# Kernel optimization log

Hardware: AMD Instinct MI355X
Metric: run time of the kernel (lower is better)

The kernel has to match this reference:

```python
import jax, jax.numpy as jnp
import numpy as np
from jax import lax

DIM = 64
B, H, W = 4, 256, 256


def setup_inputs() -> dict:
    key = jax.random.key(0)
    ks = jax.random.split(key, 6)
    d = DIM
    x = jax.random.normal(ks[0], (B, d, H, W), dtype=jnp.float32)
    w_hidden = jax.random.normal(ks[1], (6 * d, d), dtype=jnp.float32) * 0.05      # 1x1 conv dim->6*dim
    w_dw = jax.random.normal(ks[2], (6 * d, 1, 3, 3), dtype=jnp.float32) * 0.05    # depthwise 3x3
    norm_w = jnp.ones((2 * d,), dtype=jnp.float32)
    norm_b = jnp.zeros((2 * d,), dtype=jnp.float32)
    w_out = jax.random.normal(ks[3], (d, 2 * d), dtype=jnp.float32) * 0.05         # 1x1 conv 2*dim->dim
    return {"x": x, "w_hidden": w_hidden, "w_dw": w_dw,
            "norm_w": norm_w, "norm_b": norm_b, "w_out": w_out, "patch_size": 8}


def reference(x, w_hidden, w_dw, norm_w, norm_b, w_out, patch_size):
    p = patch_size
    b, c, h, w = x.shape
    # 1x1 conv: dim -> 6*dim
    hidden = jnp.einsum('oc,bchw->bohw', w_hidden, x)
    # depthwise 3x3 conv, padding=1
    hidden = lax.conv_general_dilated(
        hidden, w_dw, window_strides=(1, 1), padding='SAME',
        dimension_numbers=('NCHW', 'OIHW', 'NCHW'),
        feature_group_count=w_dw.shape[0])
    q, k, v = jnp.split(hidden, 3, axis=1)  # each [b, 2c, h, w]

    c2 = 2 * c
    def to_patch(t):  # b c (h p1) (w p2) -> b c h w p1 p2
        return t.reshape(b, c2, h // p, p, w // p, p).transpose(0, 1, 2, 4, 3, 5)

    q_fft = jnp.fft.rfft2(to_patch(q).astype(jnp.float32))
    k_fft = jnp.fft.rfft2(to_patch(k).astype(jnp.float32))
    out = jnp.fft.irfft2(q_fft * k_fft, s=(p, p))  # circular conv per patch
    # b c h w p1 p2 -> b c (h p1) (w p2)
    out = out.transpose(0, 1, 2, 4, 3, 5).reshape(b, c2, h, w)

    # WithBias LayerNorm over channel dim (to_3d normalizes last dim = channels)
    mu = out.mean(axis=1, keepdims=True)
    var = out.var(axis=1, keepdims=True)
    out_norm = (out - mu) / jnp.sqrt(var + 1e-5)
    out_norm = out_norm * norm_w[None, :, None, None] + norm_b[None, :, None, None]

    gated = v * out_norm
    # 1x1 conv: 2*dim -> dim
    return jnp.einsum('oc,bchw->bohw', w_out, gated)
```

## Files before the change

kernel.cpp:

```cpp
#include <hip/hip_runtime.h>


typedef _Float16 f16x8 __attribute__((ext_vector_type(8)));
typedef _Float16 f16x4 __attribute__((ext_vector_type(4)));
typedef _Float16 f16x2 __attribute__((ext_vector_type(2)));
typedef __fp16   h16x2 __attribute__((ext_vector_type(2)));
typedef float    f32x4 __attribute__((ext_vector_type(4)));

#define XS_OFF    0
#define HS_OFF    12800
#define QCC_OFF   25600
#define TMP_OFF   43008
#define MU_OFF    51712
#define RSTD_OFF  51968
#define LNW_OFF   52224
#define LNB_OFF   52480
#define LDS_BYTES 52736

__global__ __launch_bounds__(512, 4) void lfsa_fused(
    const float* __restrict__ x,
    const float* __restrict__ wh,
    const float* __restrict__ wdw,
    const float* __restrict__ nw,
    const float* __restrict__ nb,
    const float* __restrict__ wo,
    float* __restrict__ out)
{
    extern __shared__ char lds[];
    _Float16* xs    = (_Float16*)(lds + XS_OFF);
    _Float16* hs    = (_Float16*)(lds + HS_OFF);
    _Float16* qcc16 = (_Float16*)(lds + QCC_OFF);
    _Float16* tmp16 = (_Float16*)(lds + TMP_OFF);
    _Float16* gs16  = (_Float16*)(lds + TMP_OFF);
    float*    scrF  = (float*)(lds + TMP_OFF);
    float*    mu_s  = (float*)(lds + MU_OFF);
    float*    rstd_s= (float*)(lds + RSTD_OFF);
    _Float16* lnw16 = (_Float16*)(lds + LNW_OFF);
    _Float16* lnb16 = (_Float16*)(lds + LNB_OFF);

    const int tid = threadIdx.x;
    const int px = blockIdx.x, py = blockIdx.y, bz = blockIdx.z;
    const int lane = tid & 63;
    const int wv   = tid >> 6;
    const int m16  = lane & 15;
    const int quad = lane >> 4;

    {
        const int pix  = tid & 127;
        const int gg   = tid >> 7;
        const int prow = pix / 10;
        const int pcol = pix - prow * 10;
        const int yy = py * 8 + prow - 1;
        const int xx = px * 8 + pcol - 1;
        const bool inimg = (pix < 100) && ((unsigned)yy < 256u) && ((unsigned)xx < 256u);
        if (pix < 100) {
            const float* xp = inimg
                ? (x + (size_t)((bz * 64 + gg * 16) * 65536 + yy * 256 + xx)) : x;
            f16x8 lo, hi;
            #pragma unroll
            for (int i = 0; i < 8; ++i) {
                lo[i] = (_Float16)(inimg ? xp[(size_t)i * 65536] : 0.0f);
                hi[i] = (_Float16)(inimg ? xp[(size_t)(i + 8) * 65536] : 0.0f);
            }
            const int s = pix & 7;
            _Float16* xrow = xs + pix * 64;
            *(f16x8*)(xrow + (((2 * gg)     ^ s) * 8)) = lo;
            *(f16x8*)(xrow + (((2 * gg + 1) ^ s) * 8)) = hi;
        }
        if (tid < 128) { lnw16[tid] = (_Float16)nw[tid]; lnb16[tid] = (_Float16)nb[tid]; }
    }

    const int dwo = tid >> 3;
    const int blk = tid & 7;
    const int by2 = (blk >> 1) * 2;
    const int bx4 = (blk & 1) * 4;
    const int ci  = tid & 7;

    const int ot = wv >> 1;
    const float* wha = wh + (size_t)(ot * 16 + m16) * 64 + quad * 8;
    float4 wr0 = *(const float4*)(wha);
    float4 wr1 = *(const float4*)(wha + 4);
    float4 wr2 = *(const float4*)(wha + 32);
    float4 wr3 = *(const float4*)(wha + 36);

    f32x4 pacc2[2] = {{0.f,0.f,0.f,0.f},{0.f,0.f,0.f,0.f}};
    float sS2[8], sQ2[8];

    __syncthreads();

    #pragma unroll 1
    for (int kc = 0; kc < 6; ++kc) {
        const f16x8 a0 = {(_Float16)wr0.x,(_Float16)wr0.y,(_Float16)wr0.z,(_Float16)wr0.w,
                          (_Float16)wr1.x,(_Float16)wr1.y,(_Float16)wr1.z,(_Float16)wr1.w};
        const f16x8 a1 = {(_Float16)wr2.x,(_Float16)wr2.y,(_Float16)wr2.z,(_Float16)wr2.w,
                          (_Float16)wr3.x,(_Float16)wr3.y,(_Float16)wr3.z,(_Float16)wr3.w};
        if (kc < 5) {
            const float* nx = wha + (size_t)(kc + 1) * 4096;
            wr0 = *(const float4*)(nx);
            wr1 = *(const float4*)(nx + 4);
            wr2 = *(const float4*)(nx + 32);
            wr3 = *(const float4*)(nx + 36);
        }
        float w9c[9];
        #pragma unroll
        for (int t = 0; t < 9; ++t) w9c[t] = wdw[(kc * 64 + dwo) * 9 + t];

        {
            const int np  = (wv & 1) ? 3 : 4;
            const int pt0 = (wv & 1) * 4;
            for (int pp = 0; pp < np; ++pp) {
                const int pt = pt0 + pp;
                const int pixg = pt * 16 + m16;
                const _Float16* xrow = xs + pixg * 64;
                const int c0 = ((quad ^ (pixg & 7)) * 8);
                const f16x8 b0 = *(const f16x8*)(xrow + c0);
                const f16x8 b1 = *(const f16x8*)(xrow + (c0 ^ 32));
                f32x4 d = {0.f,0.f,0.f,0.f};
                d = __builtin_amdgcn_mfma_f32_16x16x32_f16(b0, a0, d, 0, 0, 0);
                d = __builtin_amdgcn_mfma_f32_16x16x32_f16(b1, a1, d, 0, 0, 0);
                const int pbase = pt * 16 + quad * 4;
                if (pbase < 100) {
                    *(f16x4*)(hs + 100 * (ot * 16 + m16) + pbase) =
                        f16x4{(_Float16)d[0], (_Float16)d[1],
                              (_Float16)d[2], (_Float16)d[3]};
                }
            }
        }
        __syncthreads();

        if (kc == 4) {
            if (tid < 64) {
                float S = 0.0f, Q = 0.0f;
                #pragma unroll
                for (int w = 0; w < 8; ++w) {
                    S += scrF[272 * w + tid];
                    Q += scrF[272 * w + 64 + tid];
                }
                const float sm = S * 0.0078125f;
                const float sq = Q * 0.0078125f;
                mu_s[tid]   = sm;
                rstd_s[tid] = rsqrtf(sq - sm * sm + 1e-5f);
            }
            __syncthreads();
        }

        if (kc < 4) {
            const _Float16* hrow = hs + 100 * dwo;
            float in[4][6];
            #pragma unroll
            for (int r = 0; r < 4; ++r) {
                const _Float16* rp = hrow + (by2 + r) * 10 + bx4;
                const f16x2 p0 = *(const f16x2*)rp;
                const f16x2 p1 = *(const f16x2*)(rp + 2);
                const f16x2 p2 = *(const f16x2*)(rp + 4);
                in[r][0] = (float)p0[0]; in[r][1] = (float)p0[1];
                in[r][2] = (float)p1[0]; in[r][3] = (float)p1[1];
                in[r][4] = (float)p2[0]; in[r][5] = (float)p2[1];
            }
            #pragma unroll
            for (int r = 0; r < 2; ++r) {
                float rv[4];
                #pragma unroll
                for (int c = 0; c < 4; ++c) {
                    float s = 0.0f;
                    #pragma unroll
                    for (int dy = 0; dy < 3; ++dy)
                        #pragma unroll
                        for (int dx = 0; dx < 3; ++dx)
                            s = fmaf(w9c[dy * 3 + dx], in[r + dy][c + dx], s);
                    rv[c] = s;
                }
                const int off = (by2 + r) * 8 + bx4;
                _Float16* dst = (kc < 2) ? (qcc16 + 68 * (kc * 64 + dwo))
                                         : (tmp16 + 68 * dwo);
                *(f16x4*)(dst + off) = f16x4{(_Float16)rv[0], (_Float16)rv[1],
                                             (_Float16)rv[2], (_Float16)rv[3]};
            }
        } else {
            const _Float16* hrow = hs + 100 * dwo;
            const int chg = (kc - 4) * 64 + dwo;
            const float lw = (float)lnw16[chg], lb = (float)lnb16[chg];
            const _Float16* ccrow = qcc16 + 68 * chg;
            float in[4][6];
            #pragma unroll
            for (int r = 0; r < 4; ++r) {
                const _Float16* rp = hrow + (by2 + r) * 10 + bx4;
                const f16x2 p0 = *(const f16x2*)rp;
                const f16x2 p1 = *(const f16x2*)(rp + 2);
                const f16x2 p2 = *(const f16x2*)(rp + 4);
                in[r][0] = (float)p0[0]; in[r][1] = (float)p0[1];
                in[r][2] = (float)p1[0]; in[r][3] = (float)p1[1];
                in[r][4] = (float)p2[0]; in[r][5] = (float)p2[1];
            }
            #pragma unroll
            for (int r = 0; r < 2; ++r) {
                const int prow = by2 + r;
                const f16x4 cc4 = *(const f16x4*)(ccrow + prow * 8 + bx4);
                const f32x4 mu4 = *(const f32x4*)(mu_s + prow * 8 + bx4);
                const f32x4 rs4 = *(const f32x4*)(rstd_s + prow * 8 + bx4);
                #pragma unroll
                for (int c = 0; c < 4; ++c) {
                    float s = 0.0f;
                    #pragma unroll
                    for (int dy = 0; dy < 3; ++dy)
                        #pragma unroll
                        for (int dx = 0; dx < 3; ++dx)
                            s = fmaf(w9c[dy * 3 + dx], in[r + dy][c + dx], s);
                    const float nrm = ((float)cc4[c] - mu4[c]) * rs4[c] * lw + lb;
                    gs16[(prow * 8 + bx4 + c) * 68 + dwo] = (_Float16)(s * nrm);
                }
            }
        }
        __syncthreads();

        if (kc == 2 || kc == 3) {
            const int ch = (kc - 2) * 64 + dwo;
            _Float16* qrow = qcc16 + 68 * ch;
            const _Float16* krow = tmp16 + 68 * dwo;
            float acc[8];
            #pragma unroll
            for (int j = 0; j < 8; ++j) acc[j] = 0.0f;
            #pragma unroll
            for (int a = 0; a < 8; ++a) {
                const f16x8 qv = *(const f16x8*)(qrow + 8 * a);
                h16x2 q2[4];
                #pragma unroll
                for (int t = 0; t < 4; ++t) {
                    q2[t][0] = (__fp16)qv[2 * t];
                    q2[t][1] = (__fp16)qv[2 * t + 1];
                }
                const int r = (ci - a) & 7;
                const f16x8 kr = *(const f16x8*)(krow + 8 * r);
                h16x2 rp[8];
                #pragma unroll
                for (int i = 0; i < 8; ++i)
                    rp[i] = h16x2{(__fp16)kr[i], (__fp16)kr[(i + 7) & 7]};
                #pragma unroll
                for (int j = 0; j < 8; ++j)
                    #pragma unroll
                    for (int t = 0; t < 4; ++t)
                        acc[j] = __builtin_amdgcn_fdot2(q2[t], rp[(j - 2 * t) & 7],
                                                        acc[j], false);
            }
            #pragma unroll
            for (int j = 0; j < 8; ++j) {
                float sS = acc[j];
                float sQ = acc[j] * acc[j];
                sS += __shfl_xor(sS, 8, 64);
                sQ += __shfl_xor(sQ, 8, 64);
                sS += __shfl_xor(sS, 16, 64);
                sQ += __shfl_xor(sQ, 16, 64);
                sS += __shfl_xor(sS, 32, 64);
                sQ += __shfl_xor(sQ, 32, 64);
                if (kc == 2) { sS2[j] = sS; sQ2[j] = sQ; }
                else         { sS2[j] += sS; sQ2[j] += sQ; }
            }
            *(f16x4*)(qrow + 8 * ci)     = f16x4{(_Float16)acc[0], (_Float16)acc[1],
                                                 (_Float16)acc[2], (_Float16)acc[3]};
            *(f16x4*)(qrow + 8 * ci + 4) = f16x4{(_Float16)acc[4], (_Float16)acc[5],
                                                 (_Float16)acc[6], (_Float16)acc[7]};
            if (kc == 3 && lane < 8) {
                float* w0 = scrF + 272 * wv + lane * 8;
                *(f32x4*)(w0)          = f32x4{sS2[0], sS2[1], sS2[2], sS2[3]};
                *(f32x4*)(w0 + 4)      = f32x4{sS2[4], sS2[5], sS2[6], sS2[7]};
                *(f32x4*)(w0 + 64)     = f32x4{sQ2[0], sQ2[1], sQ2[2], sQ2[3]};
                *(f32x4*)(w0 + 68)     = f32x4{sQ2[4], sQ2[5], sQ2[6], sQ2[7]};
            }
        }

        if (kc >= 4) {
            const int cb = (kc - 4) * 64;
            const float* wop = wo + (size_t)(ot * 16 + m16) * 128 + cb + quad * 8;
            const float4 u0 = *(const float4*)(wop);
            const float4 u1 = *(const float4*)(wop + 4);
            const float4 u2 = *(const float4*)(wop + 32);
            const float4 u3 = *(const float4*)(wop + 36);
            const f16x8 pa0 = {(_Float16)u0.x,(_Float16)u0.y,(_Float16)u0.z,(_Float16)u0.w,
                               (_Float16)u1.x,(_Float16)u1.y,(_Float16)u1.z,(_Float16)u1.w};
            const f16x8 pa1 = {(_Float16)u2.x,(_Float16)u2.y,(_Float16)u2.z,(_Float16)u2.w,
                               (_Float16)u3.x,(_Float16)u3.y,(_Float16)u3.z,(_Float16)u3.w};
            #pragma unroll
            for (int tt = 0; tt < 2; ++tt) {
                const int pt = (wv & 1) * 2 + tt;
                const _Float16* bp = gs16 + (pt * 16 + m16) * 68 + quad * 8;
                const f16x8 b0 = *(const f16x8*)bp;
                const f16x8 b1 = *(const f16x8*)(bp + 32);
                pacc2[tt] = __builtin_amdgcn_mfma_f32_16x16x32_f16(pa0, b0, pacc2[tt], 0, 0, 0);
                pacc2[tt] = __builtin_amdgcn_mfma_f32_16x16x32_f16(pa1, b1, pacc2[tt], 0, 0, 0);
            }
        }
    }

    {
        #pragma unroll
        for (int tt = 0; tt < 2; ++tt) {
            const int pixg = ((wv & 1) * 2 + tt) * 16 + m16;
            const int r = pixg >> 3, c = pixg & 7;
            float* op = out + (size_t)(bz * 64 + ot * 16 + quad * 4) * 65536
                            + (py * 8 + r) * 256 + px * 8 + c;
            #pragma unroll
            for (int reg = 0; reg < 4; ++reg)
                op[(size_t)reg * 65536] = pacc2[tt][reg];
        }
    }
}

extern "C" void kernel_launch(void* const* d_in, const int* in_sizes, int n_in,
                              void* d_out, int out_size, void* d_ws, size_t ws_size,
                              hipStream_t stream) {
    const float* x   = (const float*)d_in[0];
    const float* wh  = (const float*)d_in[1];
    const float* wdw = (const float*)d_in[2];
    const float* nw  = (const float*)d_in[3];
    const float* nb  = (const float*)d_in[4];
    const float* wo  = (const float*)d_in[5];
    float* outp = (float*)d_out;

    (void)hipFuncSetAttribute((const void*)lfsa_fused,
                              hipFuncAttributeMaxDynamicSharedMemorySize, LDS_BYTES);
    dim3 grid(32, 32, 4);
    lfsa_fused<<<grid, 512, LDS_BYTES, stream>>>(x, wh, wdw, nw, nb, wo, outp);
}
```

Baseline: 398.7 us.

## Hoist x fragments into registers and alias xs with qcc to shrink LDS

Loads the per-wave x B-fragments from LDS once before the kc loop and keeps them in registers, so the x staging buffer can share space with the qcc buffer. The LDS layout is repacked, cutting the per-block footprint, which may allow more resident blocks per CU. The weight prefetch across iterations is dropped in favor of in-loop loads. The cost is more VGPRs per thread and exposed global weight-load latency.

```diff
diff --git a/kernel.cpp b/kernel.cpp
--- a/kernel.cpp
+++ b/kernel.cpp
@@ -7,15 +7,14 @@
 typedef __fp16   h16x2 __attribute__((ext_vector_type(2)));
 typedef float    f32x4 __attribute__((ext_vector_type(4)));
 
-#define XS_OFF    0
-#define HS_OFF    12800
-#define QCC_OFF   25600
-#define TMP_OFF   43008
-#define MU_OFF    51712
-#define RSTD_OFF  51968
-#define LNW_OFF   52224
-#define LNB_OFF   52480
-#define LDS_BYTES 52736
+#define QCC_OFF   0
+#define TMP_OFF   17408
+#define HS_OFF    26112
+#define MU_OFF    38912
+#define RSTD_OFF  39168
+#define LNW_OFF   39424
+#define LNB_OFF   39680
+#define LDS_BYTES 39936
 
 __global__ __launch_bounds__(512, 4) void lfsa_fused(
     const float* __restrict__ x,
@@ -27,12 +26,12 @@
     float* __restrict__ out)
 {
     extern __shared__ char lds[];
-    _Float16* xs    = (_Float16*)(lds + XS_OFF);
-    _Float16* hs    = (_Float16*)(lds + HS_OFF);
+    _Float16* xs    = (_Float16*)(lds + QCC_OFF);
     _Float16* qcc16 = (_Float16*)(lds + QCC_OFF);
     _Float16* tmp16 = (_Float16*)(lds + TMP_OFF);
     _Float16* gs16  = (_Float16*)(lds + TMP_OFF);
     float*    scrF  = (float*)(lds + TMP_OFF);
+    _Float16* hs    = (_Float16*)(lds + HS_OFF);
     float*    mu_s  = (float*)(lds + MU_OFF);
     float*    rstd_s= (float*)(lds + RSTD_OFF);
     _Float16* lnw16 = (_Float16*)(lds + LNW_OFF);
@@ -78,52 +77,51 @@
 
     const int ot = wv >> 1;
     const float* wha = wh + (size_t)(ot * 16 + m16) * 64 + quad * 8;
-    float4 wr0 = *(const float4*)(wha);
-    float4 wr1 = *(const float4*)(wha + 4);
-    float4 wr2 = *(const float4*)(wha + 32);
-    float4 wr3 = *(const float4*)(wha + 36);
 
     f32x4 pacc2[2] = {{0.f,0.f,0.f,0.f},{0.f,0.f,0.f,0.f}};
     float sS2[8], sQ2[8];
 
     __syncthreads();
 
+    const int np  = (wv & 1) ? 3 : 4;
+    const int pt0 = (wv & 1) * 4;
+    f16x8 xb0[4], xb1[4];
+    #pragma unroll
+    for (int pp = 0; pp < 4; ++pp) {
+        const int pixg = (pt0 + ((pp < np) ? pp : 0)) * 16 + m16;
+        const _Float16* xrow = xs + pixg * 64;
+        const int c0 = ((quad ^ (pixg & 7)) * 8);
+        xb0[pp] = *(const f16x8*)(xrow + c0);
+        xb1[pp] = *(const f16x8*)(xrow + (c0 ^ 32));
+    }
+
     #pragma unroll 1
     for (int kc = 0; kc < 6; ++kc) {
-        const f16x8 a0 = {(_Float16)wr0.x,(_Float16)wr0.y,(_Float16)wr0.z,(_Float16)wr0.w,
-                          (_Float16)wr1.x,(_Float16)wr1.y,(_Float16)wr1.z,(_Float16)wr1.w};
-        const f16x8 a1 = {(_Float16)wr2.x,(_Float16)wr2.y,(_Float16)wr2.z,(_Float16)wr2.w,
-                          (_Float16)wr3.x,(_Float16)wr3.y,(_Float16)wr3.z,(_Float16)wr3.w};
-        if (kc < 5) {
-            const float* nx = wha + (size_t)(kc + 1) * 4096;
-            wr0 = *(const float4*)(nx);
-            wr1 = *(const float4*)(nx + 4);
-            wr2 = *(const float4*)(nx + 32);
-            wr3 = *(const float4*)(nx + 36);
-        }
+        const float* wp = wha + (size_t)kc * 4096;
+        const float4 v0 = *(const float4*)(wp);
+        const float4 v1 = *(const float4*)(wp + 4);
+        const float4 v2 = *(const float4*)(wp + 32);
+        const float4 v3 = *(const float4*)(wp + 36);
         float w9c[9];
         #pragma unroll
         for (int t = 0; t < 9; ++t) w9c[t] = wdw[(kc * 64 + dwo) * 9 + t];
-
-        {
-            const int np  = (wv & 1) ? 3 : 4;
-            const int pt0 = (wv & 1) * 4;
-            for (int pp = 0; pp < np; ++pp) {
-                const int pt = pt0 + pp;
-                const int pixg = pt * 16 + m16;
-                const _Float16* xrow = xs + pixg * 64;
-                const int c0 = ((quad ^ (pixg & 7)) * 8);
-                const f16x8 b0 = *(const f16x8*)(xrow + c0);
-                const f16x8 b1 = *(const f16x8*)(xrow + (c0 ^ 32));
-                f32x4 d = {0.f,0.f,0.f,0.f};
-                d = __builtin_amdgcn_mfma_f32_16x16x32_f16(b0, a0, d, 0, 0, 0);
-                d = __builtin_amdgcn_mfma_f32_16x16x32_f16(b1, a1, d, 0, 0, 0);
-                const int pbase = pt * 16 + quad * 4;
-                if (pbase < 100) {
-                    *(f16x4*)(hs + 100 * (ot * 16 + m16) + pbase) =
-                        f16x4{(_Float16)d[0], (_Float16)d[1],
-                              (_Float16)d[2], (_Float16)d[3]};
-                }
+        const f16x8 a0 = {(_Float16)v0.x,(_Float16)v0.y,(_Float16)v0.z,(_Float16)v0.w,
+                          (_Float16)v1.x,(_Float16)v1.y,(_Float16)v1.z,(_Float16)v1.w};
+        const f16x8 a1 = {(_Float16)v2.x,(_Float16)v2.y,(_Float16)v2.z,(_Float16)v2.w,
+                          (_Float16)v3.x,(_Float16)v3.y,(_Float16)v3.z,(_Float16)v3.w};
+
+        #pragma unroll
+        for (int pp = 0; pp < 4; ++pp) {
+            if (pp >= np) break;
+            const int pt = pt0 + pp;
+            f32x4 d = {0.f,0.f,0.f,0.f};
+            d = __builtin_amdgcn_mfma_f32_16x16x32_f16(xb0[pp], a0, d, 0, 0, 0);
+            d = __builtin_amdgcn_mfma_f32_16x16x32_f16(xb1[pp], a1, d, 0, 0, 0);
+            const int pbase = pt * 16 + quad * 4;
+            if (pbase < 100) {
+                *(f16x4*)(hs + 100 * (ot * 16 + m16) + pbase) =
+                    f16x4{(_Float16)d[0], (_Float16)d[1],
+                          (_Float16)d[2], (_Float16)d[3]};
             }
         }
         __syncthreads();
```

Measured after the change: 492.4 us. 1.23x slower.

## Double-buffer hidden tile and pipeline next-chunk GEMM with current depthwise stage

Applied to the files above, without the earlier changes.

The hidden-activation LDS buffer becomes two buffers. The 1x1-conv MFMA for channel chunk kc+1 is issued in the same barrier interval as the depthwise and elementwise work for chunk kc. The gated output gets two separate buffers, and its projection is deferred so one __syncthreads per iteration can go. This aims to cut barrier stalls and overlap matrix-core work with VALU work. In exchange, LDS use rises from about 52KB to about 74KB per block, which may lower how many blocks fit on a CU.

```diff
diff --git a/kernel.cpp b/kernel.cpp
--- a/kernel.cpp
+++ b/kernel.cpp
@@ -8,14 +8,16 @@
 typedef float    f32x4 __attribute__((ext_vector_type(4)));
 
 #define XS_OFF    0
-#define HS_OFF    12800
-#define QCC_OFF   25600
-#define TMP_OFF   43008
-#define MU_OFF    51712
-#define RSTD_OFF  51968
-#define LNW_OFF   52224
-#define LNB_OFF   52480
-#define LDS_BYTES 52736
+#define QCC_OFF   12800
+#define GS0_OFF   30208
+#define TMP_OFF   38912
+#define HS0_OFF   47616
+#define HS1_OFF   60416
+#define MU_OFF    73216
+#define RSTD_OFF  73472
+#define LNW_OFF   73728
+#define LNB_OFF   73984
+#define LDS_BYTES 74240
 
 __global__ __launch_bounds__(512, 4) void lfsa_fused(
     const float* __restrict__ x,
@@ -28,10 +30,10 @@
 {
     extern __shared__ char lds[];
     _Float16* xs    = (_Float16*)(lds + XS_OFF);
-    _Float16* hs    = (_Float16*)(lds + HS_OFF);
     _Float16* qcc16 = (_Float16*)(lds + QCC_OFF);
+    _Float16* gs0   = (_Float16*)(lds + GS0_OFF);
     _Float16* tmp16 = (_Float16*)(lds + TMP_OFF);
-    _Float16* gs16  = (_Float16*)(lds + TMP_OFF);
+    _Float16* gs1   = (_Float16*)(lds + TMP_OFF);
     float*    scrF  = (float*)(lds + TMP_OFF);
     float*    mu_s  = (float*)(lds + MU_OFF);
     float*    rstd_s= (float*)(lds + RSTD_OFF);
@@ -44,6 +46,22 @@
     const int wv   = tid >> 6;
     const int m16  = lane & 15;
     const int quad = lane >> 4;
+
+    const int dwo = tid >> 3;
+    const int blk = tid & 7;
+    const int by2 = (blk >> 1) * 2;
+    const int bx4 = (blk & 1) * 4;
+    const int ci  = tid & 7;
+
+    const int ot = wv >> 1;
+    const float* wha = wh + (size_t)(ot * 16 + m16) * 64 + quad * 8;
+    const int np  = (wv & 1) ? 3 : 4;
+    const int pt0 = (wv & 1) * 4;
+
+    float4 wr0 = *(const float4*)(wha);
+    float4 wr1 = *(const float4*)(wha + 4);
+    float4 wr2 = *(const float4*)(wha + 32);
+    float4 wr3 = *(const float4*)(wha + 36);
 
     {
         const int pix  = tid & 127;
@@ -70,63 +88,87 @@
         if (tid < 128) { lnw16[tid] = (_Float16)nw[tid]; lnb16[tid] = (_Float16)nb[tid]; }
     }
 
-    const int dwo = tid >> 3;
-    const int blk = tid & 7;
-    const int by2 = (blk >> 1) * 2;
-    const int bx4 = (blk & 1) * 4;
-    const int ci  = tid & 7;
-
-    const int ot = wv >> 1;
-    const float* wha = wh + (size_t)(ot * 16 + m16) * 64 + quad * 8;
-    float4 wr0 = *(const float4*)(wha);
-    float4 wr1 = *(const float4*)(wha + 4);
-    float4 wr2 = *(const float4*)(wha + 32);
-    float4 wr3 = *(const float4*)(wha + 36);
-
     f32x4 pacc2[2] = {{0.f,0.f,0.f,0.f},{0.f,0.f,0.f,0.f}};
     float sS2[8], sQ2[8];
 
+    auto do_gemm = [&](f16x8 a0, f16x8 a1, _Float16* hsbuf) {
+        for (int pp = 0; pp < np; ++pp) {
+            const int pt = pt0 + pp;
+            const int pixg = pt * 16 + m16;
+            const _Float16* xrow = xs + pixg * 64;
+            const int c0 = ((quad ^ (pixg & 7)) * 8);
+            const f16x8 b0 = *(const f16x8*)(xrow + c0);
+            const f16x8 b1 = *(const f16x8*)(xrow + (c0 ^ 32));
+            f32x4 d = {0.f,0.f,0.f,0.f};
+            d = __builtin_amdgcn_mfma_f32_16x16x32_f16(b0, a0, d, 0, 0, 0);
+            d = __builtin_amdgcn_mfma_f32_16x16x32_f16(b1, a1, d, 0, 0, 0);
+            const int pbase = pt * 16 + quad * 4;
+            if (pbase < 100) {
+                *(f16x4*)(hsbuf + 100 * (ot * 16 + m16) + pbase) =
+                    f16x4{(_Float16)d[0], (_Float16)d[1],
+                          (_Float16)d[2], (_Float16)d[3]};
+            }
+        }
+    };
+
+    auto do_proj = [&](const _Float16* gsbuf, int cb) {
+        const float* wop = wo + (size_t)(ot * 16 + m16) * 128 + cb + quad * 8;
+        const float4 u0 = *(const float4*)(wop);
+        const float4 u1 = *(const float4*)(wop + 4);
+        const float4 u2 = *(const float4*)(wop + 32);
+        const float4 u3 = *(const float4*)(wop + 36);
+        const f16x8 pa0 = {(_Float16)u0.x,(_Float16)u0.y,(_Float16)u0.z,(_Float16)u0.w,
+                           (_Float16)u1.x,(_Float16)u1.y,(_Float16)u1.z,(_Float16)u1.w};
+        const f16x8 pa1 = {(_Float16)u2.x,(_Float16)u2.y,(_Float16)u2.z,(_Float16)u2.w,
+                           (_Float16)u3.x,(_Float16)u3.y,(_Float16)u3.z,(_Float16)u3.w};
+        #pragma unroll
+        for (int tt = 0; tt < 2; ++tt) {
+            const int pt = (wv & 1) * 2 + tt;
+            const _Float16* bp = gsbuf + (pt * 16 + m16) * 68 + quad * 8;
+            const f16x8 b0 = *(const f16x8*)bp;
+            const f16x8 b1 = *(const f16x8*)(bp + 32);
+            pacc2[tt] = __builtin_amdgcn_mfma_f32_16x16x32_f16(pa0, b0, pacc2[tt], 0, 0, 0);
+            pacc2[tt] = __builtin_amdgcn_mfma_f32_16x16x32_f16(pa1, b1, pacc2[tt], 0, 0, 0);
+        }
+    };
+
     __syncthreads();
 
-    #pragma unroll 1
-    for (int kc = 0; kc < 6; ++kc) {
+    {
         const f16x8 a0 = {(_Float16)wr0.x,(_Float16)wr0.y,(_Float16)wr0.z,(_Float16)wr0.w,
                           (_Float16)wr1.x,(_Float16)wr1.y,(_Float16)wr1.z,(_Float16)wr1.w};
         const f16x8 a1 = {(_Float16)wr2.x,(_Float16)wr2.y,(_Float16)wr2.z,(_Float16)wr2.w,
                           (_Float16)wr3.x,(_Float16)wr3.y,(_Float16)wr3.z,(_Float16)wr3.w};
-        if (kc < 5) {
-            const float* nx = wha + (size_t)(kc + 1) * 4096;
-            wr0 = *(const float4*)(nx);
-            wr1 = *(const float4*)(nx + 4);
-            wr2 = *(const float4*)(nx + 32);
-            wr3 = *(const float4*)(nx + 36);
-        }
+        const float* nx = wha + 4096;
+        wr0 = *(const float4*)(nx);
+        wr1 = *(const float4*)(nx + 4);
+        wr2 = *(const float4*)(nx + 32);
+        wr3 = *(const float4*)(nx + 36);
+        do_gemm(a0, a1, (_Float16*)(lds + HS0_OFF));
+    }
+
+    #pragma unroll 1
+    for (int kc = 0; kc < 6; ++kc) {
+        __syncthreads();
+
         float w9c[9];
         #pragma unroll
         for (int t = 0; t < 9; ++t) w9c[t] = wdw[(kc * 64 + dwo) * 9 + t];
 
-        {
-            const int np  = (wv & 1) ? 3 : 4;
-            const int pt0 = (wv & 1) * 4;
-            for (int pp = 0; pp < np; ++pp) {
-                const int pt = pt0 + pp;
-                const int pixg = pt * 16 + m16;
-                const _Float16* xrow = xs + pixg * 64;
-                const int c0 = ((quad ^ (pixg & 7)) * 8);
-                const f16x8 b0 = *(const f16x8*)(xrow + c0);
-                const f16x8 b1 = *(const f16x8*)(xrow + (c0 ^ 32));
-                f32x4 d = {0.f,0.f,0.f,0.f};
-                d = __builtin_amdgcn_mfma_f32_16x16x32_f16(b0, a0, d, 0, 0, 0);
-                d = __builtin_amdgcn_mfma_f32_16x16x32_f16(b1, a1, d, 0, 0, 0);
-                const int pbase = pt * 16 + quad * 4;
-                if (pbase < 100) {
-                    *(f16x4*)(hs + 100 * (ot * 16 + m16) + pbase) =
-                        f16x4{(_Float16)d[0], (_Float16)d[1],
-                              (_Float16)d[2], (_Float16)d[3]};
-                }
-            }
-        }
-        __syncthreads();
+        if (kc < 5) {
+            const f16x8 a0 = {(_Float16)wr0.x,(_Float16)wr0.y,(_Float16)wr0.z,(_Float16)wr0.w,
+                              (_Float16)wr1.x,(_Float16)wr1.y,(_Float16)wr1.z,(_Float16)wr1.w};
+            const f16x8 a1 = {(_Float16)wr2.x,(_Float16)wr2.y,(_Float16)wr2.z,(_Float16)wr2.w,
+                              (_Float16)wr3.x,(_Float16)wr3.y,(_Float16)wr3.z,(_Float16)wr3.w};
+            if (kc < 4) {
+                const float* nx = wha + (size_t)(kc + 2) * 4096;
+                wr0 = *(const float4*)(nx);
+                wr1 = *(const float4*)(nx + 4);
+                wr2 = *(const float4*)(nx + 32);
+                wr3 = *(const float4*)(nx + 36);
+            }
+            do_gemm(a0, a1, (_Float16*)(lds + (((kc + 1) & 1) ? HS1_OFF : HS0_OFF)));
+        }
 
         if (kc == 4) {
             if (tid < 64) {
@@ -144,8 +186,10 @@
             __syncthreads();
         }
 
+        const _Float16* hcur = (_Float16*)(lds + ((kc & 1) ? HS1_OFF : HS0_OFF));
+
         if (kc < 4) {
-            const _Float16* hrow = hs + 100 * dwo;
+            const _Float16* hrow = hcur + 100 * dwo;
             float in[4][6];
             #pragma unroll
             for (int r = 0; r < 4; ++r) {
@@ -177,10 +221,11 @@
                                              (_Float16)rv[2], (_Float16)rv[3]};
             }
         } else {
-            const _Float16* hrow = hs + 100 * dwo;
+            const _Float16* hrow = hcur + 100 * dwo;
             const int chg = (kc - 4) * 64 + dwo;
             const float lw = (float)lnw16[chg], lb = (float)lnb16[chg];
             const _Float16* ccrow = qcc16 + 68 * chg;
+            _Float16* gsc = (kc == 4) ? gs0 : gs1;
             float in[4][6];
             #pragma unroll
             for (int r = 0; r < 4; ++r) {
@@ -207,11 +252,10 @@
                         for (int dx = 0; dx < 3; ++dx)
                             s = fmaf(w9c[dy * 3 + dx], in[r + dy][c + dx], s);
                     const float nrm = ((float)cc4[c] - mu4[c]) * rs4[c] * lw + lb;
-                    gs16[(prow * 8 + bx4 + c) * 68 + dwo] = (_Float16)(s * nrm);
+                    gsc[(prow * 8 + bx4 + c) * 68 + dwo] = (_Float16)(s * nrm);
                 }
             }
         }
-        __syncthreads();
 
         if (kc == 2 || kc == 3) {
             const int ch = (kc - 2) * 64 + dwo;
@@ -268,28 +312,14 @@
             }
         }
 
-        if (kc >= 4) {
-            const int cb = (kc - 4) * 64;
-            const float* wop = wo + (size_t)(ot * 16 + m16) * 128 + cb + quad * 8;
-            const float4 u0 = *(const float4*)(wop);
-            const float4 u1 = *(const float4*)(wop + 4);
-            const float4 u2 = *(const float4*)(wop + 32);
-            const float4 u3 = *(const float4*)(wop + 36);
-            const f16x8 pa0 = {(_Float16)u0.x,(_Float16)u0.y,(_Float16)u0.z,(_Float16)u0.w,
-                               (_Float16)u1.x,(_Float16)u1.y,(_Float16)u1.z,(_Float16)u1.w};
-            const f16x8 pa1 = {(_Float16)u2.x,(_Float16)u2.y,(_Float16)u2.z,(_Float16)u2.w,
-                               (_Float16)u3.x,(_Float16)u3.y,(_Float16)u3.z,(_Float16)u3.w};
-            #pragma unroll
-            for (int tt = 0; tt < 2; ++tt) {
-                const int pt = (wv & 1) * 2 + tt;
-                const _Float16* bp = gs16 + (pt * 16 + m16) * 68 + quad * 8;
-                const f16x8 b0 = *(const f16x8*)bp;
-                const f16x8 b1 = *(const f16x8*)(bp + 32);
-                pacc2[tt] = __builtin_amdgcn_mfma_f32_16x16x32_f16(pa0, b0, pacc2[tt], 0, 0, 0);
-                pacc2[tt] = __builtin_amdgcn_mfma_f32_16x16x32_f16(pa1, b1, pacc2[tt], 0, 0, 0);
-            }
+        if (kc == 5) {
+            do_proj(gs0, 0);
         }
     }
+
+    __syncthreads();
+
+    do_proj(gs1, 64);
 
     {
         #pragma unroll
```

Measured after the change: 399.3 us. About the same (+0.2%).

## Process 128 hidden channels per round to halve barrier-separated stages

Applied to the files above, without the earlier changes.

Restructures the six 64-channel stages into three 128-channel rounds: each wave computes a full 16-channel MFMA tile over all pixel tiles, and the depthwise, circular-convolution and gating steps each handle two channels per thread. This cuts the number of barriers and loop iterations and batches the output projection into one round. In exchange, LDS use grows from about 52KB to about 74KB, which may limit how many 512-thread blocks fit per CU (launch bounds ask for 4), and register pressure rises from the doubled weights and unrolled work.

```diff
diff --git a/kernel.cpp b/kernel.cpp
--- a/kernel.cpp
+++ b/kernel.cpp
@@ -9,13 +9,13 @@
 
 #define XS_OFF    0
 #define HS_OFF    12800
-#define QCC_OFF   25600
-#define TMP_OFF   43008
-#define MU_OFF    51712
-#define RSTD_OFF  51968
-#define LNW_OFF   52224
-#define LNB_OFF   52480
-#define LDS_BYTES 52736
+#define QCC_OFF   38400
+#define TMP_OFF   55808
+#define MU_OFF    73216
+#define RSTD_OFF  73472
+#define LNW_OFF   73728
+#define LNB_OFF   73984
+#define LDS_BYTES 74240
 
 __global__ __launch_bounds__(512, 4) void lfsa_fused(
     const float* __restrict__ x,
@@ -45,6 +45,21 @@
     const int m16  = lane & 15;
     const int quad = lane >> 4;
 
+    const int dwo = tid >> 3;
+    const int blk = tid & 7;
+    const int by2 = (blk >> 1) * 2;
+    const int bx4 = (blk & 1) * 4;
+    const int ci  = tid & 7;
+
+    const int och = wv * 16 + m16;
+    const float* wha = wh + (size_t)och * 64 + quad * 8;
+    const int ot  = wv >> 1;
+
+    float4 wr0 = *(const float4*)(wha);
+    float4 wr1 = *(const float4*)(wha + 4);
+    float4 wr2 = *(const float4*)(wha + 32);
+    float4 wr3 = *(const float4*)(wha + 36);
+
     {
         const int pix  = tid & 127;
         const int gg   = tid >> 7;
@@ -70,65 +85,49 @@
         if (tid < 128) { lnw16[tid] = (_Float16)nw[tid]; lnb16[tid] = (_Float16)nb[tid]; }
     }
 
-    const int dwo = tid >> 3;
-    const int blk = tid & 7;
-    const int by2 = (blk >> 1) * 2;
-    const int bx4 = (blk & 1) * 4;
-    const int ci  = tid & 7;
-
-    const int ot = wv >> 1;
-    const float* wha = wh + (size_t)(ot * 16 + m16) * 64 + quad * 8;
-    float4 wr0 = *(const float4*)(wha);
-    float4 wr1 = *(const float4*)(wha + 4);
-    float4 wr2 = *(const float4*)(wha + 32);
-    float4 wr3 = *(const float4*)(wha + 36);
-
     f32x4 pacc2[2] = {{0.f,0.f,0.f,0.f},{0.f,0.f,0.f,0.f}};
-    float sS2[8], sQ2[8];
 
     __syncthreads();
 
     #pragma unroll 1
-    for (int kc = 0; kc < 6; ++kc) {
+    for (int rg = 0; rg < 3; ++rg) {
         const f16x8 a0 = {(_Float16)wr0.x,(_Float16)wr0.y,(_Float16)wr0.z,(_Float16)wr0.w,
                           (_Float16)wr1.x,(_Float16)wr1.y,(_Float16)wr1.z,(_Float16)wr1.w};
         const f16x8 a1 = {(_Float16)wr2.x,(_Float16)wr2.y,(_Float16)wr2.z,(_Float16)wr2.w,
                           (_Float16)wr3.x,(_Float16)wr3.y,(_Float16)wr3.z,(_Float16)wr3.w};
-        if (kc < 5) {
-            const float* nx = wha + (size_t)(kc + 1) * 4096;
+        if (rg < 2) {
+            const float* nx = wha + (size_t)(rg + 1) * 8192;
             wr0 = *(const float4*)(nx);
             wr1 = *(const float4*)(nx + 4);
             wr2 = *(const float4*)(nx + 32);
             wr3 = *(const float4*)(nx + 36);
         }
-        float w9c[9];
+        float w9a[9], w9b[9];
         #pragma unroll
-        for (int t = 0; t < 9; ++t) w9c[t] = wdw[(kc * 64 + dwo) * 9 + t];
-
-        {
-            const int np  = (wv & 1) ? 3 : 4;
-            const int pt0 = (wv & 1) * 4;
-            for (int pp = 0; pp < np; ++pp) {
-                const int pt = pt0 + pp;
-                const int pixg = pt * 16 + m16;
-                const _Float16* xrow = xs + pixg * 64;
-                const int c0 = ((quad ^ (pixg & 7)) * 8);
-                const f16x8 b0 = *(const f16x8*)(xrow + c0);
-                const f16x8 b1 = *(const f16x8*)(xrow + (c0 ^ 32));
-                f32x4 d = {0.f,0.f,0.f,0.f};
-                d = __builtin_amdgcn_mfma_f32_16x16x32_f16(b0, a0, d, 0, 0, 0);
-                d = __builtin_amdgcn_mfma_f32_16x16x32_f16(b1, a1, d, 0, 0, 0);
-                const int pbase = pt * 16 + quad * 4;
-                if (pbase < 100) {
-                    *(f16x4*)(hs + 100 * (ot * 16 + m16) + pbase) =
-                        f16x4{(_Float16)d[0], (_Float16)d[1],
-                              (_Float16)d[2], (_Float16)d[3]};
-                }
+        for (int t = 0; t < 9; ++t) {
+            w9a[t] = wdw[(rg * 128 + dwo) * 9 + t];
+            w9b[t] = wdw[(rg * 128 + 64 + dwo) * 9 + t];
+        }
+
+        for (int pt = 0; pt < 7; ++pt) {
+            const int pixg = pt * 16 + m16;
+            const _Float16* xrow = xs + pixg * 64;
+            const int c0 = ((quad ^ (pixg & 7)) * 8);
+            const f16x8 b0 = *(const f16x8*)(xrow + c0);
+            const f16x8 b1 = *(const f16x8*)(xrow + (c0 ^ 32));
+            f32x4 d = {0.f,0.f,0.f,0.f};
+            d = __builtin_amdgcn_mfma_f32_16x16x32_f16(b0, a0, d, 0, 0, 0);
+            d = __builtin_amdgcn_mfma_f32_16x16x32_f16(b1, a1, d, 0, 0, 0);
+            const int pbase = pt * 16 + quad * 4;
+            if (pbase < 100) {
+                *(f16x4*)(hs + 100 * och + pbase) =
+                    f16x4{(_Float16)d[0], (_Float16)d[1],
+                          (_Float16)d[2], (_Float16)d[3]};
             }
         }
         __syncthreads();
 
-        if (kc == 4) {
+        if (rg == 2) {
             if (tid < 64) {
                 float S = 0.0f, Q = 0.0f;
                 #pragma unroll
@@ -144,122 +143,138 @@
             __syncthreads();
         }
 
-        if (kc < 4) {
-            const _Float16* hrow = hs + 100 * dwo;
-            float in[4][6];
-            #pragma unroll
-            for (int r = 0; r < 4; ++r) {
-                const _Float16* rp = hrow + (by2 + r) * 10 + bx4;
-                const f16x2 p0 = *(const f16x2*)rp;
-                const f16x2 p1 = *(const f16x2*)(rp + 2);
-                const f16x2 p2 = *(const f16x2*)(rp + 4);
-                in[r][0] = (float)p0[0]; in[r][1] = (float)p0[1];
-                in[r][2] = (float)p1[0]; in[r][3] = (float)p1[1];
-                in[r][4] = (float)p2[0]; in[r][5] = (float)p2[1];
-            }
-            #pragma unroll
-            for (int r = 0; r < 2; ++r) {
-                float rv[4];
-                #pragma unroll
-                for (int c = 0; c < 4; ++c) {
-                    float s = 0.0f;
-                    #pragma unroll
-                    for (int dy = 0; dy < 3; ++dy)
+        if (rg < 2) {
+            _Float16* dstbase = (rg == 0) ? qcc16 : tmp16;
+            #pragma unroll
+            for (int h = 0; h < 2; ++h) {
+                const int chl = h * 64 + dwo;
+                const _Float16* hrow = hs + 100 * chl;
+                float in[4][6];
+                #pragma unroll
+                for (int r = 0; r < 4; ++r) {
+                    const _Float16* rp = hrow + (by2 + r) * 10 + bx4;
+                    const f16x2 p0 = *(const f16x2*)rp;
+                    const f16x2 p1 = *(const f16x2*)(rp + 2);
+                    const f16x2 p2 = *(const f16x2*)(rp + 4);
+                    in[r][0] = (float)p0[0]; in[r][1] = (float)p0[1];
+                    in[r][2] = (float)p1[0]; in[r][3] = (float)p1[1];
+                    in[r][4] = (float)p2[0]; in[r][5] = (float)p2[1];
+                }
+                #pragma unroll
+                for (int r = 0; r < 2; ++r) {
+                    float rv[4];
+                    #pragma unroll
+                    for (int c = 0; c < 4; ++c) {
+                        float s = 0.0f;
                         #pragma unroll
-                        for (int dx = 0; dx < 3; ++dx)
-                            s = fmaf(w9c[dy * 3 + dx], in[r + dy][c + dx], s);
-                    rv[c] = s;
-                }
-                const int off = (by2 + r) * 8 + bx4;
-                _Float16* dst = (kc < 2) ? (qcc16 + 68 * (kc * 64 + dwo))
-                                         : (tmp16 + 68 * dwo);
-                *(f16x4*)(dst + off) = f16x4{(_Float16)rv[0], (_Float16)rv[1],
-                                             (_Float16)rv[2], (_Float16)rv[3]};
+                        for (int dy = 0; dy < 3; ++dy)
+                            #pragma unroll
+                            for (int dx = 0; dx < 3; ++dx)
+                                s = fmaf(h ? w9b[dy * 3 + dx] : w9a[dy * 3 + dx],
+                                         in[r + dy][c + dx], s);
+                        rv[c] = s;
+                    }
+                    const int off = (by2 + r) * 8 + bx4;
+                    *(f16x4*)(dstbase + 68 * chl + off) =
+                        f16x4{(_Float16)rv[0], (_Float16)rv[1],
+                              (_Float16)rv[2], (_Float16)rv[3]};
+                }
             }
         } else {
-            const _Float16* hrow = hs + 100 * dwo;
-            const int chg = (kc - 4) * 64 + dwo;
-            const float lw = (float)lnw16[chg], lb = (float)lnb16[chg];
-            const _Float16* ccrow = qcc16 + 68 * chg;
-            float in[4][6];
-            #pragma unroll
-            for (int r = 0; r < 4; ++r) {
-                const _Float16* rp = hrow + (by2 + r) * 10 + bx4;
-                const f16x2 p0 = *(const f16x2*)rp;
-                const f16x2 p1 = *(const f16x2*)(rp + 2);
-                const f16x2 p2 = *(const f16x2*)(rp + 4);
-                in[r][0] = (float)p0[0]; in[r][1] = (float)p0[1];
-                in[r][2] = (float)p1[0]; in[r][3] = (float)p1[1];
-                in[r][4] = (float)p2[0]; in[r][5] = (float)p2[1];
-            }
-            #pragma unroll
-            for (int r = 0; r < 2; ++r) {
-                const int prow = by2 + r;
-                const f16x4 cc4 = *(const f16x4*)(ccrow + prow * 8 + bx4);
-                const f32x4 mu4 = *(const f32x4*)(mu_s + prow * 8 + bx4);
-                const f32x4 rs4 = *(const f32x4*)(rstd_s + prow * 8 + bx4);
-                #pragma unroll
-                for (int c = 0; c < 4; ++c) {
-                    float s = 0.0f;
-                    #pragma unroll
-                    for (int dy = 0; dy < 3; ++dy)
+            const f32x4 mu40 = *(const f32x4*)(mu_s + by2 * 8 + bx4);
+            const f32x4 rs40 = *(const f32x4*)(rstd_s + by2 * 8 + bx4);
+            const f32x4 mu41 = *(const f32x4*)(mu_s + (by2 + 1) * 8 + bx4);
+            const f32x4 rs41 = *(const f32x4*)(rstd_s + (by2 + 1) * 8 + bx4);
+            #pragma unroll
+            for (int h = 0; h < 2; ++h) {
+                const int chl = h * 64 + dwo;
+                const float lw = (float)lnw16[chl], lb = (float)lnb16[chl];
+                const _Float16* ccrow = qcc16 + 68 * chl;
+                const _Float16* hrow = hs + 100 * chl;
+                float in[4][6];
+                #pragma unroll
+                for (int r = 0; r < 4; ++r) {
+                    const _Float16* rp = hrow + (by2 + r) * 10 + bx4;
+                    const f16x2 p0 = *(const f16x2*)rp;
+                    const f16x2 p1 = *(const f16x2*)(rp + 2);
+                    const f16x2 p2 = *(const f16x2*)(rp + 4);
+                    in[r][0] = (float)p0[0]; in[r][1] = (float)p0[1];
+                    in[r][2] = (float)p1[0]; in[r][3] = (float)p1[1];
+                    in[r][4] = (float)p2[0]; in[r][5] = (float)p2[1];
+                }
+                #pragma unroll
+                for (int r = 0; r < 2; ++r) {
+                    const int prow = by2 + r;
+                    const f16x4 cc4 = *(const f16x4*)(ccrow + prow * 8 + bx4);
+                    const f32x4 mu4 = r ? mu41 : mu40;
+                    const f32x4 rs4 = r ? rs41 : rs40;
+                    #pragma unroll
+                    for (int c = 0; c < 4; ++c) {
+                        float s = 0.0f;
                         #pragma unroll
-                        for (int dx = 0; dx < 3; ++dx)
-                            s = fmaf(w9c[dy * 3 + dx], in[r + dy][c + dx], s);
-                    const float nrm = ((float)cc4[c] - mu4[c]) * rs4[c] * lw + lb;
-                    gs16[(prow * 8 + bx4 + c) * 68 + dwo] = (_Float16)(s * nrm);
+                        for (int dy = 0; dy < 3; ++dy)
+                            #pragma unroll
+                            for (int dx = 0; dx < 3; ++dx)
+                                s = fmaf(h ? w9b[dy * 3 + dx] : w9a[dy * 3 + dx],
+                                         in[r + dy][c + dx], s);
+                        const float nrm = ((float)cc4[c] - mu4[c]) * rs4[c] * lw + lb;
+                        gs16[(prow * 8 + bx4 + c) * 136 + chl] = (_Float16)(s * nrm);
+                    }
                 }
             }
         }
         __syncthreads();
 
-        if (kc == 2 || kc == 3) {
-            const int ch = (kc - 2) * 64 + dwo;
-            _Float16* qrow = qcc16 + 68 * ch;
-            const _Float16* krow = tmp16 + 68 * dwo;
-            float acc[8];
-            #pragma unroll
-            for (int j = 0; j < 8; ++j) acc[j] = 0.0f;
-            #pragma unroll
-            for (int a = 0; a < 8; ++a) {
-                const f16x8 qv = *(const f16x8*)(qrow + 8 * a);
-                h16x2 q2[4];
-                #pragma unroll
-                for (int t = 0; t < 4; ++t) {
-                    q2[t][0] = (__fp16)qv[2 * t];
-                    q2[t][1] = (__fp16)qv[2 * t + 1];
-                }
-                const int r = (ci - a) & 7;
-                const f16x8 kr = *(const f16x8*)(krow + 8 * r);
-                h16x2 rp[8];
-                #pragma unroll
-                for (int i = 0; i < 8; ++i)
-                    rp[i] = h16x2{(__fp16)kr[i], (__fp16)kr[(i + 7) & 7]};
-                #pragma unroll
-                for (int j = 0; j < 8; ++j)
-                    #pragma unroll
-                    for (int t = 0; t < 4; ++t)
-                        acc[j] = __builtin_amdgcn_fdot2(q2[t], rp[(j - 2 * t) & 7],
-                                                        acc[j], false);
-            }
-            #pragma unroll
-            for (int j = 0; j < 8; ++j) {
-                float sS = acc[j];
-                float sQ = acc[j] * acc[j];
-                sS += __shfl_xor(sS, 8, 64);
-                sQ += __shfl_xor(sQ, 8, 64);
-                sS += __shfl_xor(sS, 16, 64);
-                sQ += __shfl_xor(sQ, 16, 64);
-                sS += __shfl_xor(sS, 32, 64);
-                sQ += __shfl_xor(sQ, 32, 64);
-                if (kc == 2) { sS2[j] = sS; sQ2[j] = sQ; }
-                else         { sS2[j] += sS; sQ2[j] += sQ; }
-            }
-            *(f16x4*)(qrow + 8 * ci)     = f16x4{(_Float16)acc[0], (_Float16)acc[1],
-                                                 (_Float16)acc[2], (_Float16)acc[3]};
-            *(f16x4*)(qrow + 8 * ci + 4) = f16x4{(_Float16)acc[4], (_Float16)acc[5],
-                                                 (_Float16)acc[6], (_Float16)acc[7]};
-            if (kc == 3 && lane < 8) {
+        if (rg == 1) {
+            float sS2[8], sQ2[8];
+            #pragma unroll
+            for (int cch = 0; cch < 2; ++cch) {
+                _Float16* qrow = qcc16 + 68 * (cch * 64 + dwo);
+                const _Float16* krow = tmp16 + 68 * (cch * 64 + dwo);
+                float acc[8];
+                #pragma unroll
+                for (int j = 0; j < 8; ++j) acc[j] = 0.0f;
+                #pragma unroll
+                for (int a = 0; a < 8; ++a) {
+                    const f16x8 qv = *(const f16x8*)(qrow + 8 * a);
+                    h16x2 q2[4];
+                    #pragma unroll
+                    for (int t = 0; t < 4; ++t) {
+                        q2[t][0] = (__fp16)qv[2 * t];
+                        q2[t][1] = (__fp16)qv[2 * t + 1];
+                    }
+                    const int r = (ci - a) & 7;
+                    const f16x8 kr = *(const f16x8*)(krow + 8 * r);
+                    h16x2 rp[8];
+                    #pragma unroll
+                    for (int i = 0; i < 8; ++i)
+                        rp[i] = h16x2{(__fp16)kr[i], (__fp16)kr[(i + 7) & 7]};
+                    #pragma unroll
+                    for (int j = 0; j < 8; ++j)
+                        #pragma unroll
+                        for (int t = 0; t < 4; ++t)
+                            acc[j] = __builtin_amdgcn_fdot2(q2[t], rp[(j - 2 * t) & 7],
+                                                            acc[j], false);
+                }
+                #pragma unroll
+                for (int j = 0; j < 8; ++j) {
+                    float sS = acc[j];
+                    float sQ = acc[j] * acc[j];
+                    sS += __shfl_xor(sS, 8, 64);
+                    sQ += __shfl_xor(sQ, 8, 64);
+                    sS += __shfl_xor(sS, 16, 64);
+                    sQ += __shfl_xor(sQ, 16, 64);
+                    sS += __shfl_xor(sS, 32, 64);
+                    sQ += __shfl_xor(sQ, 32, 64);
+                    if (cch == 0) { sS2[j] = sS; sQ2[j] = sQ; }
+                    else          { sS2[j] += sS; sQ2[j] += sQ; }
+                }
+                *(f16x4*)(qrow + 8 * ci)     = f16x4{(_Float16)acc[0], (_Float16)acc[1],
+                                                     (_Float16)acc[2], (_Float16)acc[3]};
+                *(f16x4*)(qrow + 8 * ci + 4) = f16x4{(_Float16)acc[4], (_Float16)acc[5],
+                                                     (_Float16)acc[6], (_Float16)acc[7]};
+            }
+            if (lane < 8) {
                 float* w0 = scrF + 272 * wv + lane * 8;
                 *(f32x4*)(w0)          = f32x4{sS2[0], sS2[1], sS2[2], sS2[3]};
                 *(f32x4*)(w0 + 4)      = f32x4{sS2[4], sS2[5], sS2[6], sS2[7]};
@@ -268,25 +283,28 @@
             }
         }
 
-        if (kc >= 4) {
-            const int cb = (kc - 4) * 64;
-            const float* wop = wo + (size_t)(ot * 16 + m16) * 128 + cb + quad * 8;
-            const float4 u0 = *(const float4*)(wop);
-            const float4 u1 = *(const float4*)(wop + 4);
-            const float4 u2 = *(const float4*)(wop + 32);
-            const float4 u3 = *(const float4*)(wop + 36);
-            const f16x8 pa0 = {(_Float16)u0.x,(_Float16)u0.y,(_Float16)u0.z,(_Float16)u0.w,
-                               (_Float16)u1.x,(_Float16)u1.y,(_Float16)u1.z,(_Float16)u1.w};
-            const f16x8 pa1 = {(_Float16)u2.x,(_Float16)u2.y,(_Float16)u2.z,(_Float16)u2.w,
-                               (_Float16)u3.x,(_Float16)u3.y,(_Float16)u3.z,(_Float16)u3.w};
-            #pragma unroll
-            for (int tt = 0; tt < 2; ++tt) {
-                const int pt = (wv & 1) * 2 + tt;
-                const _Float16* bp = gs16 + (pt * 16 + m16) * 68 + quad * 8;
-                const f16x8 b0 = *(const f16x8*)bp;
-                const f16x8 b1 = *(const f16x8*)(bp + 32);
-                pacc2[tt] = __builtin_amdgcn_mfma_f32_16x16x32_f16(pa0, b0, pacc2[tt], 0, 0, 0);
-                pacc2[tt] = __builtin_amdgcn_mfma_f32_16x16x32_f16(pa1, b1, pacc2[tt], 0, 0, 0);
+        if (rg == 2) {
+            #pragma unroll
+            for (int cch = 0; cch < 2; ++cch) {
+                const int cb = cch * 64;
+                const float* wop = wo + (size_t)(ot * 16 + m16) * 128 + cb + quad * 8;
+                const float4 u0 = *(const float4*)(wop);
+                const float4 u1 = *(const float4*)(wop + 4);
+                const float4 u2 = *(const float4*)(wop + 32);
+                const float4 u3 = *(const float4*)(wop + 36);
+                const f16x8 pa0 = {(_Float16)u0.x,(_Float16)u0.y,(_Float16)u0.z,(_Float16)u0.w,
+                                   (_Float16)u1.x,(_Float16)u1.y,(_Float16)u1.z,(_Float16)u1.w};
+                const f16x8 pa1 = {(_Float16)u2.x,(_Float16)u2.y,(_Float16)u2.z,(_Float16)u2.w,
+                                   (_Float16)u3.x,(_Float16)u3.y,(_Float16)u3.z,(_Float16)u3.w};
+                #pragma unroll
+                for (int tt = 0; tt < 2; ++tt) {
+                    const int pt = (wv & 1) * 2 + tt;
+                    const _Float16* bp = gs16 + (pt * 16 + m16) * 136 + cb + quad * 8;
+                    const f16x8 b0 = *(const f16x8*)bp;
+                    const f16x8 b1 = *(const f16x8*)(bp + 32);
+                    pacc2[tt] = __builtin_amdgcn_mfma_f32_16x16x32_f16(pa0, b0, pacc2[tt], 0, 0, 0);
+                    pacc2[tt] = __builtin_amdgcn_mfma_f32_16x16x32_f16(pa1, b1, pacc2[tt], 0, 0, 0);
+                }
             }
         }
     }
```

New measurement: 444.5 us. 11.5% more time.
